# Optimization experiments

Measured on AMD Instinct MI355X. Metric: run time of the kernel, lower is better.

## Reference

```python
import jax, jax.numpy as jnp
import numpy as np

B, S, D, H = 4, 2048, 512, 8
E = D // H  # d_head = 64

def setup_inputs() -> dict:
    key = jax.random.key(0)
    ks = jax.random.split(key, 10)
    s_in = (1.0 / np.sqrt(D))
    x  = jax.random.normal(ks[0], (B, S, D), dtype=jnp.float32)
    Wq = jax.random.normal(ks[1], (H, D, E), dtype=jnp.float32) * s_in
    bq = jax.random.normal(ks[2], (H, E), dtype=jnp.float32) * 0.01
    Wk = jax.random.normal(ks[3], (H, D, E), dtype=jnp.float32) * s_in
    bk = jax.random.normal(ks[4], (H, E), dtype=jnp.float32) * 0.01
    Wv = jax.random.normal(ks[5], (H, D, E), dtype=jnp.float32) * s_in
    bv = jax.random.normal(ks[6], (H, E), dtype=jnp.float32) * 0.01
    Wo = jax.random.normal(ks[7], (D, D), dtype=jnp.float32) * s_in
    bo = jax.random.normal(ks[8], (D,), dtype=jnp.float32) * 0.01
    return {"x": x, "Wq": Wq, "bq": bq, "Wk": Wk, "bk": bk,
            "Wv": Wv, "bv": bv, "Wo": Wo, "bo": bo}

def reference(x, Wq, bq, Wk, bk, Wv, bv, Wo, bo):
    B_, S_, D_ = x.shape
    # per-head projections (batched over head axis h)
    q = jnp.einsum('bsd,hde->bhse', x, Wq) + bq[None, :, None, :]
    k = jnp.einsum('bsd,hde->bhse', x, Wk) + bk[None, :, None, :]
    v = jnp.einsum('bsd,hde->bhse', x, Wv) + bv[None, :, None, :]
    # NOTE: original scales by d_model**-0.5 (full D), not d_head**-0.5
    scale = jnp.asarray(D_, x.dtype) ** -0.5
    scores = jnp.einsum('bhse,bhte->bhst', q, k) * scale  # [B,H,S,S]
    causal = jnp.tril(jnp.ones((S_, S_), dtype=bool))
    scores = jnp.where(causal[None, None], scores, -jnp.inf)
    attn = jax.nn.softmax(scores, axis=-1)
    out = jnp.einsum('bhst,bhte->bhse', attn, v)  # [B,H,S,E]
    # concat heads along feature dim (head-major), matching torch.cat
    out = out.transpose(0, 2, 1, 3).reshape(B_, S_, D_)
    return out @ Wo + bo  # final projection; dropout never applied in source
```

## Files before the change

kernel.cpp:

```cpp
#include <hip/hip_runtime.h>

typedef unsigned short u16;
typedef __bf16 bf16x8 __attribute__((ext_vector_type(8)));
typedef short s16x4 __attribute__((ext_vector_type(4)));
typedef short s16x8 __attribute__((ext_vector_type(8)));
typedef float f32x4 __attribute__((ext_vector_type(4)));

#define BB 4
#define SS 2048
#define DD 512
#define HH 8
#define EE 64
#define MM 8192
#define BHSE (BB*HH*SS*EE)

#define GLOBAL_AS __attribute__((address_space(1)))
#define LDS_AS    __attribute__((address_space(3)))

__device__ __forceinline__ float b2f(u16 u) {
    return __uint_as_float(((unsigned int)u) << 16);
}
__device__ __forceinline__ u16 f2b(float f) {
    unsigned int v = __float_as_uint(f);
    v += 0x7fffu + ((v >> 16) & 1u);
    return (u16)(v >> 16);
}
__device__ __forceinline__ float loadE(const void* p, size_t idx, int isbf16) {
    return isbf16 ? b2f(((const u16*)p)[idx]) : ((const float*)p)[idx];
}
__device__ __forceinline__ f32x4 mfma16x16x16_bf16(s16x4 a, s16x4 b, f32x4 c) {
    return __builtin_amdgcn_mfma_f32_16x16x16bf16_1k(a, b, c, 0, 0, 0);
}
__device__ __forceinline__ void load_lds16(const u16* g, u16* l) {
    __builtin_amdgcn_global_load_lds((GLOBAL_AS void*)g, (LDS_AS void*)l, 16, 0, 0);
}

__device__ __forceinline__ int detect_bf16_wave(const u16* x) {
    const int lane = threadIdx.x & 63;
    float a0 = fabsf(b2f(x[2 * lane]));
    float a1 = fabsf(b2f(x[2 * (lane + 64)]));
    int c0 = (a0 == 0.f) || (a0 > 1e-4f && a0 < 100.f);
    int c1 = (a1 == 0.f) || (a1 > 1e-4f && a1 < 100.f);
    int cnt = __popcll(__ballot(c0)) + __popcll(__ballot(c1));
    return cnt >= 96;
}

__global__ __launch_bounds__(256) void prep(
    const void* __restrict__ X,
    const void* __restrict__ Wq, const void* __restrict__ Wk,
    const void* __restrict__ Wv, const void* __restrict__ Wo,
    u16* __restrict__ Xb, u16* __restrict__ WT, u16* __restrict__ WoT,
    int* __restrict__ flag)
{
    const int isbf16 = detect_bf16_wave((const u16*)X);
    const int bid = blockIdx.x;
    const int tid = threadIdx.x;
    if (bid < 1024) {
        if (bid == 0 && tid == 0) *flag = isbf16;
        const size_t i0 = ((size_t)bid * 256 + tid) * 16;
        if (isbf16) {
            const uint4* src = (const uint4*)(((const u16*)X) + i0);
            uint4* dst = (uint4*)(Xb + i0);
            dst[0] = src[0];
            dst[1] = src[1];
        } else {
            const float* xf = ((const float*)X) + i0;
            float4 f0 = *(const float4*)xf;
            float4 f1 = *(const float4*)(xf + 4);
            float4 f2 = *(const float4*)(xf + 8);
            float4 f3 = *(const float4*)(xf + 12);
            u16 tmp[16] = { f2b(f0.x), f2b(f0.y), f2b(f0.z), f2b(f0.w),
                            f2b(f1.x), f2b(f1.y), f2b(f1.z), f2b(f1.w),
                            f2b(f2.x), f2b(f2.y), f2b(f2.z), f2b(f2.w),
                            f2b(f3.x), f2b(f3.y), f2b(f3.z), f2b(f3.w) };
            *(uint4*)(Xb + i0) = *(const uint4*)tmp;
            *(uint4*)(Xb + i0 + 8) = *(const uint4*)(tmp + 8);
        }
        return;
    }
    const int j = bid - 1024;
    const int job = j >> 6;
    const int t = j & 63;
    const void* src; u16* dst; int src_ld;
    if (job < 3) {
        const void* W = (job == 0) ? Wq : ((job == 1) ? Wk : Wv);
        int h = t >> 3, kt = t & 7;
        size_t off = (size_t)h * DD * EE + (size_t)kt * 64 * EE;
        src = isbf16 ? (const void*)(((const u16*)W) + off)
                     : (const void*)(((const float*)W) + off);
        src_ld = EE;
        dst = WT + (size_t)job * 512 * 512 + (size_t)(h * 64) * 512 + kt * 64;
    } else {
        int a = t >> 3, b = t & 7;
        size_t off = (size_t)(a * 64) * 512 + b * 64;
        src = isbf16 ? (const void*)(((const u16*)Wo) + off)
                     : (const void*)(((const float*)Wo) + off);
        src_ld = 512;
        dst = WoT + (size_t)(b * 64) * 512 + a * 64;
    }
    __shared__ __align__(16) u16 Ts[64 * 72];
#pragma unroll
    for (int it = 0; it < 2; ++it) {
        int idx = it * 256 + tid;
        int r = idx >> 3, c = (idx & 7) << 3;
        u16 tmp[8];
        if (isbf16) {
            *(bf16x8*)tmp = *(const bf16x8*)(((const u16*)src) + (size_t)r * src_ld + c);
        } else {
            const float* sp = ((const float*)src) + (size_t)r * src_ld + c;
            float4 f0 = *(const float4*)sp;
            float4 f1 = *(const float4*)(sp + 4);
            tmp[0] = f2b(f0.x); tmp[1] = f2b(f0.y); tmp[2] = f2b(f0.z); tmp[3] = f2b(f0.w);
            tmp[4] = f2b(f1.x); tmp[5] = f2b(f1.y); tmp[6] = f2b(f1.z); tmp[7] = f2b(f1.w);
        }
#pragma unroll
        for (int k = 0; k < 8; ++k) Ts[(c + k) * 72 + r] = tmp[k];
    }
    __syncthreads();
#pragma unroll
    for (int it = 0; it < 2; ++it) {
        int idx = it * 256 + tid;
        int r = idx >> 3, c = (idx & 7) << 3;
        *(bf16x8*)(dst + (size_t)r * 512 + c) = *(const bf16x8*)&Ts[r * 72 + c];
    }
}

template<int MT, int NT>
__device__ __forceinline__ void mfma_step(const u16* As, const u16* Bs,
    int mh, int nh, int lq, int quad, f32x4 acc[MT][NT])
{
    const int sw = lq & 7;
#pragma unroll
    for (int kw = 0; kw < 2; ++kw) {
        const int G = kw * 4 + quad;
        const int col = ((G ^ sw) << 3);
        bf16x8 a[MT], b[NT];
#pragma unroll
        for (int mt = 0; mt < MT; ++mt)
            a[mt] = *(const bf16x8*)&As[(mh + mt * 16 + lq) * 64 + col];
#pragma unroll
        for (int nt = 0; nt < NT; ++nt)
            b[nt] = *(const bf16x8*)&Bs[(nh + nt * 16 + lq) * 64 + col];
#pragma unroll
        for (int mt = 0; mt < MT; ++mt)
#pragma unroll
            for (int nt = 0; nt < NT; ++nt)
                acc[mt][nt] = __builtin_amdgcn_mfma_f32_16x16x32_bf16(a[mt], b[nt], acc[mt][nt], 0, 0, 0);
    }
}

__global__ __launch_bounds__(256) void gemm_qkv(
    const u16* __restrict__ Xb, const u16* __restrict__ WT,
    const void* __restrict__ bq, const void* __restrict__ bk,
    const void* __restrict__ bv, u16* __restrict__ qkv,
    const int* __restrict__ flag)
{
    const float SCALE2 = 0.06376741654380187f;
    const int isbf16 = *flag;
    const int l = blockIdx.x;
    const int m0 = ((l & 7) * 8 + ((l >> 3) & 7)) * 128;
    const int n0 = (l >> 6) * 128;
    const int tid = threadIdx.x;
    const int wave = tid >> 6, lane = tid & 63;
    const int lq = lane & 15, quad = lane >> 4;
    const int mh = (wave & 1) * 64, nh = (wave >> 1) * 64;
    __shared__ __align__(16) u16 As[128 * 64];
    __shared__ __align__(16) u16 Bs[128 * 64];
    f32x4 acc[4][4] = {};

    const int swz = (lane & 7) ^ ((lane >> 3) & 7);
    const size_t lane_off = (size_t)(lane >> 3) * 512 + 8 * swz;

    for (int k0 = 0; k0 < 512; k0 += 64) {
        __syncthreads();
#pragma unroll
        for (int jj = 0; jj < 4; ++jj) {
            const int c = wave * 4 + jj;
            load_lds16(Xb + (size_t)(m0 + 8 * c) * 512 + k0 + lane_off, &As[c * 512]);
            load_lds16(WT + (size_t)(n0 + 8 * c) * 512 + k0 + lane_off, &Bs[c * 512]);
        }
        __syncthreads();
        mfma_step<4, 4>(As, Bs, mh, nh, lq, quad, acc);
    }

    const int proj = n0 >> 9;
    const void* bias = (proj == 0) ? bq : ((proj == 1) ? bk : bv);
#pragma unroll
    for (int mt = 0; mt < 4; ++mt) {
#pragma unroll
        for (int nt = 0; nt < 4; ++nt) {
#pragma unroll
            for (int r = 0; r < 4; ++r) {
                int m = m0 + mh + mt * 16 + quad * 4 + r;
                int n = n0 + nh + nt * 16 + lq;
                int nn = n & 511;
                float v = acc[mt][nt][r] + loadE(bias, nn, isbf16);
                if (proj == 0) v *= SCALE2;
                int b_ = m >> 11, s = m & 2047, h = nn >> 6, e = nn & 63;
                qkv[(size_t)proj * BHSE + (((size_t)(b_ * HH + h) * SS + s) * EE + e)] = f2b(v);
            }
        }
    }
}

struct Stage { uint4 k0, k1, va, vb; };

__device__ __forceinline__ void stage_load(Stage& st, const u16* Kh, const u16* Vh,
                                           int t0, int tid) {
    int r = tid >> 3, c = (tid & 7) * 8;
    st.k0 = *(const uint4*)(Kh + (size_t)(t0 + r) * 64 + c);
    st.k1 = *(const uint4*)(Kh + (size_t)(t0 + r + 32) * 64 + c);
    int t2 = 2 * (tid & 31), e8 = (tid >> 5) * 8;
    st.va = *(const uint4*)(Vh + (size_t)(t0 + t2) * 64 + e8);
    st.vb = *(const uint4*)(Vh + (size_t)(t0 + t2 + 1) * 64 + e8);
}
__device__ __forceinline__ void stage_write(const Stage& st, u16* Ksb, u16* VTsb, int tid) {
    int r = tid >> 3, c = (tid & 7) * 8;
    *(uint4*)(Ksb + r * 72 + c) = st.k0;
    *(uint4*)(Ksb + (r + 32) * 72 + c) = st.k1;
    int t2 = 2 * (tid & 31), e8 = (tid >> 5) * 8;
    int g2 = ((t2 >> 2) & 3) * 16 + ((t2 >> 4) << 2) + (t2 & 3);
    const unsigned* pa = (const unsigned*)&st.va;
    const unsigned* pb = (const unsigned*)&st.vb;
#pragma unroll
    for (int k = 0; k < 4; ++k) {
        unsigned lo = __builtin_amdgcn_perm(pb[k], pa[k], 0x05040100u);
        unsigned hi = __builtin_amdgcn_perm(pb[k], pa[k], 0x07060302u);
        *(unsigned*)(VTsb + (e8 + 2 * k) * 72 + g2) = lo;
        *(unsigned*)(VTsb + (e8 + 2 * k + 1) * 72 + g2) = hi;
    }
}

__device__ __forceinline__ void attn_tile(const u16* Ksb, const u16* VTsb,
    bf16x8 qf0, bf16x8 qf1, int lq, int quad, int wave, bool diag,
    f32x4 Ot[4], f32x4& lfrag)
{
    const s16x4 ones = { (short)0x3F80, (short)0x3F80, (short)0x3F80, (short)0x3F80 };
#pragma unroll
    for (int half = 0; half < 2; ++half) {
        s16x4 vf[4][2];
#pragma unroll
        for (int et = 0; et < 4; ++et) {
            const u16* Vp = VTsb + (et * 16 + lq) * 72 + quad * 16 + half * 8;
            s16x8 v = *(const s16x8*)Vp;
            vf[et][0] = __builtin_shufflevector(v, v, 0, 1, 2, 3);
            vf[et][1] = __builtin_shufflevector(v, v, 4, 5, 6, 7);
        }
#pragma unroll
        for (int tj = 0; tj < 2; ++tj) {
            const int tt = half * 2 + tj;
            const u16* Krow = Ksb + (tt * 16 + lq) * 72;
            bf16x8 k0 = *(const bf16x8*)(Krow + quad * 8);
            bf16x8 k1 = *(const bf16x8*)(Krow + 32 + quad * 8);
            f32x4 sc = {};
            sc = __builtin_amdgcn_mfma_f32_16x16x32_bf16(k0, qf0, sc, 0, 0, 0);
            sc = __builtin_amdgcn_mfma_f32_16x16x32_bf16(k1, qf1, sc, 0, 0, 0);
            unsigned pu[4];
#pragma unroll
            for (int r = 0; r < 4; ++r) {
                float p = exp2f(sc[r]);
                if (diag) {
                    int tl = tt * 16 + quad * 4 + r;
                    int ql = 16 * wave + lq;
                    p = (tl <= ql) ? p : 0.f;
                }
                pu[r] = __float_as_uint(p);
            }
            union { unsigned u[2]; s16x4 s; } pf;
            pf.u[0] = __builtin_amdgcn_perm(pu[1], pu[0], 0x07060302u);
            pf.u[1] = __builtin_amdgcn_perm(pu[3], pu[2], 0x07060302u);
            lfrag = mfma16x16x16_bf16(ones, pf.s, lfrag);
#pragma unroll
            for (int et = 0; et < 4; ++et)
                Ot[et] = mfma16x16x16_bf16(vf[et][tj], pf.s, Ot[et]);
        }
    }
}

__global__ __launch_bounds__(256) void attn_kernel(
    const u16* __restrict__ Qg, const u16* __restrict__ Kg,
    const u16* __restrict__ Vg, u16* __restrict__ Og)
{
    const int bh = blockIdx.x;
    const int qb = ((int)gridDim.y - 1 - (int)blockIdx.y) * 64;
    const int nt = qb >> 6;
    const int tid = threadIdx.x;
    const int wave = tid >> 6, lane = tid & 63;
    const int lq = lane & 15, quad = lane >> 4;
    const int b = bh >> 3, h = bh & 7;

    const size_t base = (size_t)bh * SS * EE;
    const u16* Kh = Kg + base;
    const u16* Vh = Vg + base;

    __shared__ __align__(16) u16 Ks[64 * 72];
    __shared__ __align__(16) u16 VTs[64 * 72];

    const int qrow = qb + 16 * wave + lq;
    const u16* Qp = Qg + base + (size_t)qrow * EE;
    bf16x8 qf0 = *(const bf16x8*)(Qp + quad * 8);
    bf16x8 qf1 = *(const bf16x8*)(Qp + 32 + quad * 8);

    f32x4 Ot[4] = {};
    f32x4 lfrag = {};

    Stage st;
    stage_load(st, Kh, Vh, 0, tid);
    stage_write(st, Ks, VTs, tid);
    for (int i = 0; i <= nt; ++i) {
        __syncthreads();
        const bool more = (i < nt);
        if (more) stage_load(st, Kh, Vh, (i + 1) * 64, tid);
        attn_tile(Ks, VTs, qf0, qf1, lq, quad, wave, i == nt, Ot, lfrag);
        __syncthreads();
        if (more) stage_write(st, Ks, VTs, tid);
    }

    const float inv = 1.f / lfrag[0];

    u16* Op = Og + (((size_t)(b * SS + qrow)) * HH + h) * EE;
#pragma unroll
    for (int et = 0; et < 4; ++et) {
        u16 tmp[4];
#pragma unroll
        for (int r = 0; r < 4; ++r) tmp[r] = f2b(Ot[et][r] * inv);
        *(uint2*)(Op + et * 16 + quad * 4) = *(const uint2*)tmp;
    }
}

__global__ __launch_bounds__(256) void gemm_out(
    const u16* __restrict__ A, const u16* __restrict__ WoT,
    const void* __restrict__ bo, void* __restrict__ out,
    const int* __restrict__ flag)
{
    const int isbf16 = *flag;
    const int l = blockIdx.x;
    const int m0 = ((l & 7) * 8 + ((l >> 3) & 7)) * 128;
    const int n0 = (l >> 6) * 64;
    const int tid = threadIdx.x;
    const int wave = tid >> 6, lane = tid & 63;
    const int lq = lane & 15, quad = lane >> 4;
    const int mh = (wave & 1) * 64, nh = (wave >> 1) * 32;
    __shared__ __align__(16) u16 As[128 * 64];
    __shared__ __align__(16) u16 Bs[64 * 64];
    f32x4 acc[4][2] = {};

    const int swz = (lane & 7) ^ ((lane >> 3) & 7);
    const size_t lane_off = (size_t)(lane >> 3) * 512 + 8 * swz;

    for (int k0 = 0; k0 < 512; k0 += 64) {
        __syncthreads();
#pragma unroll
        for (int jj = 0; jj < 4; ++jj) {
            const int c = wave * 4 + jj;
            load_lds16(A + (size_t)(m0 + 8 * c) * 512 + k0 + lane_off, &As[c * 512]);
        }
#pragma unroll
        for (int jj = 0; jj < 2; ++jj) {
            const int c = wave * 2 + jj;
            load_lds16(WoT + (size_t)(n0 + 8 * c) * 512 + k0 + lane_off, &Bs[c * 512]);
        }
        __syncthreads();
        mfma_step<4, 2>(As, Bs, mh, nh, lq, quad, acc);
    }
#pragma unroll
    for (int mt = 0; mt < 4; ++mt) {
#pragma unroll
        for (int nt = 0; nt < 2; ++nt) {
#pragma unroll
            for (int r = 0; r < 4; ++r) {
                int m = m0 + mh + mt * 16 + quad * 4 + r;
                int n = n0 + nh + nt * 16 + lq;
                float v = acc[mt][nt][r] + loadE(bo, n, isbf16);
                if (isbf16) ((u16*)out)[(size_t)m * 512 + n] = f2b(v);
                else        ((float*)out)[(size_t)m * 512 + n] = v;
            }
        }
    }
}

extern "C" void kernel_launch(void* const* d_in, const int* in_sizes, int n_in,
                              void* d_out, int out_size, void* d_ws, size_t ws_size,
                              hipStream_t stream) {
    const void* x  = d_in[0];
    const void* Wq = d_in[1];
    const void* bq = d_in[2];
    const void* Wk = d_in[3];
    const void* bk = d_in[4];
    const void* Wv = d_in[5];
    const void* bv = d_in[6];
    const void* Wo = d_in[7];
    const void* bo = d_in[8];

    u16* WT   = (u16*)d_ws;
    u16* WoT  = WT + 3 * 512 * 512;
    u16* qkv  = WoT + 512 * 512;
    u16* attn = qkv + 3 * (size_t)BHSE;
    int* flag = (int*)(attn + (size_t)BHSE);
    u16* Xb   = (u16*)(flag + 8);

    prep<<<1024 + 256, 256, 0, stream>>>(x, Wq, Wk, Wv, Wo, Xb, WT, WoT, flag);
    gemm_qkv<<<(MM / 128) * (1536 / 128), 256, 0, stream>>>(Xb, WT, bq, bk, bv, qkv, flag);
    attn_kernel<<<dim3(BB * HH, SS / 64), 256, 0, stream>>>(qkv, qkv + BHSE, qkv + 2 * (size_t)BHSE, attn);
    gemm_out<<<(MM / 128) * (512 / 64), 256, 0, stream>>>(attn, WoT, bo, d_out, flag);
}
```

Measured before the change: 191.9 us.

## Split long causal attention query tiles across two blocks with a reduction pass

The upper 16 query tiles of each head, which have the most KV tiles, are now split into two halves of the KV range handled by separate blocks. Each half writes unnormalized bf16 partial outputs and row sums to scratch, and a new reduce kernel adds them and normalizes. This is meant to balance the causal workload and shorten the critical path of the longest blocks. The cost is an extra kernel launch, scratch traffic, and bf16 rounding of the partials. It relies on no running max being needed, as in the original softmax.

```diff
diff --git a/kernel.cpp b/kernel.cpp
--- a/kernel.cpp
+++ b/kernel.cpp
@@ -279,11 +279,22 @@
 
 __global__ __launch_bounds__(256) void attn_kernel(
     const u16* __restrict__ Qg, const u16* __restrict__ Kg,
-    const u16* __restrict__ Vg, u16* __restrict__ Og)
+    const u16* __restrict__ Vg, u16* __restrict__ Og,
+    u16* __restrict__ PO, float* __restrict__ PL)
 {
     const int bh = blockIdx.x;
-    const int qb = ((int)gridDim.y - 1 - (int)blockIdx.y) * 64;
-    const int nt = qb >> 6;
+    const int z = blockIdx.y;
+    int j, i0, i1, c; bool partial;
+    if (z < 32) {
+        j = 31 - (z >> 1); c = z & 1;
+        const int ntt = j + 1, c0 = (ntt + 1) >> 1;
+        i0 = (c == 0) ? 0 : c0;
+        i1 = (c == 0) ? c0 : ntt;
+        partial = true;
+    } else {
+        j = 47 - z; c = 0; i0 = 0; i1 = j + 1; partial = false;
+    }
+    const int qb = j * 64;
     const int tid = threadIdx.x;
     const int wave = tid >> 6, lane = tid & 63;
     const int lq = lane & 15, quad = lane >> 4;
@@ -305,27 +316,62 @@
     f32x4 lfrag = {};
 
     Stage st;
-    stage_load(st, Kh, Vh, 0, tid);
+    stage_load(st, Kh, Vh, i0 * 64, tid);
     stage_write(st, Ks, VTs, tid);
-    for (int i = 0; i <= nt; ++i) {
-        __syncthreads();
-        const bool more = (i < nt);
+    for (int i = i0; i < i1; ++i) {
+        __syncthreads();
+        const bool more = (i + 1 < i1);
         if (more) stage_load(st, Kh, Vh, (i + 1) * 64, tid);
-        attn_tile(Ks, VTs, qf0, qf1, lq, quad, wave, i == nt, Ot, lfrag);
+        attn_tile(Ks, VTs, qf0, qf1, lq, quad, wave, i == j, Ot, lfrag);
         __syncthreads();
         if (more) stage_write(st, Ks, VTs, tid);
     }
 
-    const float inv = 1.f / lfrag[0];
-
-    u16* Op = Og + (((size_t)(b * SS + qrow)) * HH + h) * EE;
-#pragma unroll
-    for (int et = 0; et < 4; ++et) {
-        u16 tmp[4];
-#pragma unroll
-        for (int r = 0; r < 4; ++r) tmp[r] = f2b(Ot[et][r] * inv);
-        *(uint2*)(Op + et * 16 + quad * 4) = *(const uint2*)tmp;
-    }
+    if (!partial) {
+        const float inv = 1.f / lfrag[0];
+        u16* Op = Og + (((size_t)(b * SS + qrow)) * HH + h) * EE;
+#pragma unroll
+        for (int et = 0; et < 4; ++et) {
+            u16 tmp[4];
+#pragma unroll
+            for (int r = 0; r < 4; ++r) tmp[r] = f2b(Ot[et][r] * inv);
+            *(uint2*)(Op + et * 16 + quad * 4) = *(const uint2*)tmp;
+        }
+    } else {
+        const int slot = ((bh * 16 + (j - 16)) * 2 + c);
+        u16* Pp = PO + (size_t)slot * 4096 + (16 * wave + lq) * 64;
+#pragma unroll
+        for (int et = 0; et < 4; ++et) {
+            u16 tmp[4];
+#pragma unroll
+            for (int r = 0; r < 4; ++r) tmp[r] = f2b(Ot[et][r]);
+            *(uint2*)(Pp + et * 16 + quad * 4) = *(const uint2*)tmp;
+        }
+        if (quad == 0) PL[slot * 64 + 16 * wave + lq] = lfrag[0];
+    }
+}
+
+__global__ __launch_bounds__(256) void attn_reduce(
+    const u16* __restrict__ PO, const float* __restrict__ PL,
+    u16* __restrict__ Og)
+{
+    const int bh = blockIdx.x, jj = blockIdx.y;
+    const int j = 16 + jj;
+    const int t = threadIdx.x;
+    const int q = t >> 2, e0 = (t & 3) * 16;
+    const int slot0 = (bh * 16 + jj) * 2;
+    const u16* O0 = PO + (size_t)slot0 * 4096 + q * 64 + e0;
+    const u16* O1 = O0 + 4096;
+    const float inv = 1.f / (PL[slot0 * 64 + q] + PL[(slot0 + 1) * 64 + q]);
+    const int b = bh >> 3, h = bh & 7;
+    const int qg = j * 64 + q;
+    u16 tmp[16];
+#pragma unroll
+    for (int k = 0; k < 16; ++k)
+        tmp[k] = f2b((b2f(O0[k]) + b2f(O1[k])) * inv);
+    u16* Op = Og + (((size_t)(b * SS + qg)) * HH + h) * EE + e0;
+    *(uint4*)Op = *(const uint4*)tmp;
+    *(uint4*)(Op + 8) = *(const uint4*)(tmp + 8);
 }
 
 __global__ __launch_bounds__(256) void gemm_out(
@@ -398,9 +444,12 @@
     u16* attn = qkv + 3 * (size_t)BHSE;
     int* flag = (int*)(attn + (size_t)BHSE);
     u16* Xb   = (u16*)(flag + 8);
+    u16* PO   = Xb;
+    float* PL = (float*)(Xb + (size_t)MM * DD);
 
     prep<<<1024 + 256, 256, 0, stream>>>(x, Wq, Wk, Wv, Wo, Xb, WT, WoT, flag);
     gemm_qkv<<<(MM / 128) * (1536 / 128), 256, 0, stream>>>(Xb, WT, bq, bk, bv, qkv, flag);
-    attn_kernel<<<dim3(BB * HH, SS / 64), 256, 0, stream>>>(qkv, qkv + BHSE, qkv + 2 * (size_t)BHSE, attn);
+    attn_kernel<<<dim3(BB * HH, 48), 256, 0, stream>>>(qkv, qkv + BHSE, qkv + 2 * (size_t)BHSE, attn, PO, PL);
+    attn_reduce<<<dim3(BB * HH, 16), 256, 0, stream>>>(PO, PL, attn);
     gemm_out<<<(MM / 128) * (512 / 64), 256, 0, stream>>>(attn, WoT, bo, d_out, flag);
 }
```

New measurement: 201.6 us. 5.0% more time.
